# Kernel tuning notes

Measured on AMD Instinct MI355X. Metric: run time of the kernel, lower is better.

The kernel has to match this reference:

```python
import jax, jax.numpy as jnp
import numpy as np

LEAKY = 0.2  # tf.nn.leaky_relu default alpha
E_SZ = [64, 64, 16]
F_SZ = [128, 128, 8]
N_MAPS, C, H, W = 64, 1, 32, 32
B = 8192


def _leaky(x):
    return jnp.where(x >= 0, x, LEAKY * x)


def func_theta(x, theta, sz, in_sz):
    # x: [B, in_sz]; theta: [B, total]; per-sample MLP with weights sliced from theta
    y = x
    offset = 0
    n = len(sz)
    for i, out_sz in enumerate(sz):
        w_sz = in_sz * out_sz
        Wm = theta[:, offset:offset + w_sz].reshape(-1, in_sz, out_sz)
        offset += w_sz
        b = theta[:, offset:offset + out_sz]
        offset += out_sz
        y = jnp.einsum('bi,bio->bo', y, Wm) + b
        if i < n - 1:
            y = _leaky(y)
        in_sz = out_sz
    return y


def setup_inputs() -> dict:
    key = jax.random.key(0)
    ks = jax.random.split(key, 16)

    def g(k, shape, scale):
        return (jax.random.normal(k, shape, dtype=jnp.float32) * scale)

    inp = {
        'indices': jax.random.randint(ks[0], (B,), 0, N_MAPS, dtype=jnp.int32),
        'states': jax.random.normal(ks[1], (B, 4), dtype=jnp.float32),
        'maps': jax.random.normal(ks[2], (N_MAPS, C, H, W), dtype=jnp.float32),
        'fc1_w': g(ks[3], (C * H * W, 256), 1.0 / np.sqrt(C * H * W)),
        'fc1_b': jnp.zeros((256,), jnp.float32),
        'fc2_w': g(ks[4], (256, 128), 1.0 / np.sqrt(256)),
        'fc2_b': jnp.zeros((128,), jnp.float32),
        'fc3_w': g(ks[5], (128, 128), 1.0 / np.sqrt(128)),
        'fc3_b': jnp.zeros((128,), jnp.float32),
        'bn_w': g(ks[6], (128, 32), 1.0 / np.sqrt(128)),
        'bn_b': jnp.zeros((32,), jnp.float32),
        'e_w': g(ks[7], (32, 5456), 1e-5),
        'e_b': g(ks[8], (5456,), 1e-3),
        'f_w': g(ks[9], (32, 21768), 1e-5),
        'f_b': g(ks[10], (21768,), 1e-3),
    }
    return inp


def reference(indices, states, maps, fc1_w, fc1_b, fc2_w, fc2_b, fc3_w, fc3_b,
              bn_w, bn_b, e_w, e_b, f_w, f_b):
    # gather maps per sample and flatten (NCHW -> NHWC transpose is a no-op after flatten
    # mathematically, but keep the exact data layout of the original)
    m = jnp.transpose(maps[indices], (0, 2, 3, 1)).astype(jnp.float32)  # [B,H,W,C]
    z = m.reshape(m.shape[0], -1)

    # hypernet trunk
    z = _leaky(z @ fc1_w + fc1_b)
    z = _leaky(z @ fc2_w + fc2_b)
    z = _leaky(z @ fc3_w + fc3_b)
    z = z @ bn_w + bn_b  # bottleneck, no activation
    theta_e = z @ e_w + e_b  # [B, 5456]
    theta_f = z @ f_w + f_b  # [B, 21768]

    S = states[:, 0:2]
    G = states[:, 2:4]
    e_s = func_theta(S, theta_e, E_SZ, 2)
    e_g = func_theta(G, theta_e, E_SZ, 2)
    zf = jnp.concatenate([e_s, e_g], axis=-1)  # [B, 32]
    ang = func_theta(zf, theta_f, F_SZ, 2 * E_SZ[-1])  # [B, 8]
    pts = jnp.concatenate([jnp.sin(ang), jnp.cos(ang)], axis=-1)  # [B, 16]
    return pts
```

## Files before the change

kernel.cpp:

```cpp
#include <hip/hip_runtime.h>
#include <hip/hip_bf16.h>


#define LEAKY 0.2f
#define NCLS 64
#define B_TOT 8192
#define NSLICE 8
#define EST 68
#define FST 132


__device__ __forceinline__ float lrelu(float x) { return x >= 0.f ? x : LEAKY * x; }

__global__ __launch_bounds__(1024) void backbone_bucket_kernel(
    const float* __restrict__ maps,
    const float* __restrict__ fc1_w, const float* __restrict__ fc1_b,
    const float* __restrict__ fc2_w, const float* __restrict__ fc2_b,
    const float* __restrict__ fc3_w, const float* __restrict__ fc3_b,
    const float* __restrict__ bn_w,  const float* __restrict__ bn_b,
    float* __restrict__ z,
    const int* __restrict__ idx, int* __restrict__ counts,
    int* __restrict__ offsets, int* __restrict__ perm)
{
    __shared__ float m[1024];
    __shared__ __align__(16) float4 red4[1024];
    __shared__ __align__(16) float h1[256];
    __shared__ __align__(16) float h2[128];
    __shared__ __align__(16) float h3[128];
    __shared__ int cnt[16][64];
    __shared__ int wcur[16][64];

    const int t = threadIdx.x;

    if (blockIdx.x == 64) {
        const int w = t >> 6;
        cnt[w][t & 63] = 0;
        __syncthreads();
        int my[8];
#pragma unroll
        for (int r = 0; r < 8; ++r) {
            my[r] = idx[r * 1024 + t];
            atomicAdd(&cnt[w][my[r]], 1);
        }
        __syncthreads();
        if (t < 64) {
            int run = 0;
#pragma unroll
            for (int w2 = 0; w2 < 16; ++w2) {
                const int v = cnt[w2][t];
                wcur[w2][t] = run;
                run += v;
            }
            counts[t] = run;
            int x = run;
            for (int d = 1; d < 64; d <<= 1) {
                const int y = __shfl_up(x, d, 64);
                if (t >= d) x += y;
            }
            const int basec = x - run;
            offsets[t] = basec;
#pragma unroll
            for (int w2 = 0; w2 < 16; ++w2) wcur[w2][t] += basec;
        }
        __syncthreads();
#pragma unroll
        for (int r = 0; r < 8; ++r) {
            const int p = atomicAdd(&wcur[w][my[r]], 1);
            perm[p] = r * 1024 + t;
        }
        return;
    }

    const int c = blockIdx.x;
    m[t] = maps[(size_t)c * 1024 + t];
    __syncthreads();

    {
        const int og = t & 63, ks = t >> 6;
        const float* wp = fc1_w + og * 4;
        float4 acc = {0.f, 0.f, 0.f, 0.f};
#pragma unroll 8
        for (int i = 0; i < 64; ++i) {
            const int k = ks * 64 + i;
            const float mk = m[k];
            const float4 w = *(const float4*)&wp[(size_t)k * 256];
            acc.x += mk * w.x; acc.y += mk * w.y;
            acc.z += mk * w.z; acc.w += mk * w.w;
        }
        red4[t] = acc;
    }
    __syncthreads();
    if (t < 64) {
        float4 a = *(const float4*)&fc1_b[t * 4];
#pragma unroll
        for (int r = 0; r < 16; ++r) {
            const float4 v = red4[r * 64 + t];
            a.x += v.x; a.y += v.y; a.z += v.z; a.w += v.w;
        }
        a.x = lrelu(a.x); a.y = lrelu(a.y); a.z = lrelu(a.z); a.w = lrelu(a.w);
        *(float4*)&h1[t * 4] = a;
    }
    __syncthreads();
    {
        const int og = t & 31, ks = t >> 5;
        float4 acc = {0.f, 0.f, 0.f, 0.f};
#pragma unroll
        for (int i = 0; i < 8; ++i) {
            const int k = ks * 8 + i;
            const float hk = h1[k];
            const float4 w = *(const float4*)&fc2_w[k * 128 + og * 4];
            acc.x += hk * w.x; acc.y += hk * w.y;
            acc.z += hk * w.z; acc.w += hk * w.w;
        }
        red4[t] = acc;
    }
    __syncthreads();
    if (t < 32) {
        float4 a = *(const float4*)&fc2_b[t * 4];
#pragma unroll
        for (int r = 0; r < 32; ++r) {
            const float4 v = red4[r * 32 + t];
            a.x += v.x; a.y += v.y; a.z += v.z; a.w += v.w;
        }
        a.x = lrelu(a.x); a.y = lrelu(a.y); a.z = lrelu(a.z); a.w = lrelu(a.w);
        *(float4*)&h2[t * 4] = a;
    }
    __syncthreads();
    {
        const int og = t & 31, ks = t >> 5;
        float4 acc = {0.f, 0.f, 0.f, 0.f};
#pragma unroll
        for (int i = 0; i < 4; ++i) {
            const int k = ks * 4 + i;
            const float hk = h2[k];
            const float4 w = *(const float4*)&fc3_w[k * 128 + og * 4];
            acc.x += hk * w.x; acc.y += hk * w.y;
            acc.z += hk * w.z; acc.w += hk * w.w;
        }
        red4[t] = acc;
    }
    __syncthreads();
    if (t < 32) {
        float4 a = *(const float4*)&fc3_b[t * 4];
#pragma unroll
        for (int r = 0; r < 32; ++r) {
            const float4 v = red4[r * 32 + t];
            a.x += v.x; a.y += v.y; a.z += v.z; a.w += v.w;
        }
        a.x = lrelu(a.x); a.y = lrelu(a.y); a.z = lrelu(a.z); a.w = lrelu(a.w);
        *(float4*)&h3[t * 4] = a;
    }
    __syncthreads();
    {
        const int og = t & 7, ks = t >> 3;
        const float hk = h3[ks];
        const float4 w = *(const float4*)&bn_w[ks * 32 + og * 4];
        float4 acc;
        acc.x = hk * w.x; acc.y = hk * w.y; acc.z = hk * w.z; acc.w = hk * w.w;
        red4[t] = acc;
    }
    __syncthreads();
    if (t < 8) {
        float4 a = *(const float4*)&bn_b[t * 4];
#pragma unroll
        for (int r = 0; r < 128; ++r) {
            const float4 v = red4[r * 8 + t];
            a.x += v.x; a.y += v.y; a.z += v.z; a.w += v.w;
        }
        *(float4*)&z[c * 32 + t * 4] = a;
    }
}

__global__ __launch_bounds__(256) void theta_kernel(
    const float* __restrict__ z,
    const float* __restrict__ e_w, const float* __restrict__ e_b,
    const float* __restrict__ f_w, const float* __restrict__ f_b,
    float* __restrict__ th_e, float* __restrict__ th_f)
{
    __shared__ __align__(16) float zl[2048];
    const int t = threadIdx.x;
    ((float4*)zl)[t]       = ((const float4*)z)[t];
    ((float4*)zl)[t + 256] = ((const float4*)z)[t + 256];
    __syncthreads();

    int j = blockIdx.x * 256 + t;
    const int cbase = blockIdx.y * 8;
    const float* wbase;
    float* op;
    int stride;
    float bias;
    if (j < 5456) {
        wbase = e_w + j; bias = e_b[j]; op = th_e + j; stride = 5456;
    } else {
        const int jj = j - 5456;
        if (jj >= 21768) return;
        wbase = f_w + jj; bias = f_b[jj]; op = th_f + jj; stride = 21768;
    }
    float wk[32];
#pragma unroll
    for (int k = 0; k < 32; ++k) wk[k] = wbase[(size_t)k * stride];

#pragma unroll
    for (int cc = 0; cc < 8; cc += 4) {
        const int c0 = cbase + cc;
        float a0 = bias, a1 = bias, a2 = bias, a3 = bias;
#pragma unroll
        for (int k4 = 0; k4 < 8; ++k4) {
            const float4 z0 = *(const float4*)&zl[(c0 + 0) * 32 + k4 * 4];
            const float4 z1 = *(const float4*)&zl[(c0 + 1) * 32 + k4 * 4];
            const float4 z2 = *(const float4*)&zl[(c0 + 2) * 32 + k4 * 4];
            const float4 z3 = *(const float4*)&zl[(c0 + 3) * 32 + k4 * 4];
            const float w0 = wk[k4 * 4], w1 = wk[k4 * 4 + 1];
            const float w2 = wk[k4 * 4 + 2], w3 = wk[k4 * 4 + 3];
            a0 += z0.x * w0 + z0.y * w1 + z0.z * w2 + z0.w * w3;
            a1 += z1.x * w0 + z1.y * w1 + z1.z * w2 + z1.w * w3;
            a2 += z2.x * w0 + z2.y * w1 + z2.z * w2 + z2.w * w3;
            a3 += z3.x * w0 + z3.y * w1 + z3.z * w2 + z3.w * w3;
        }
        op[(size_t)(c0 + 0) * stride] = a0;
        op[(size_t)(c0 + 1) * stride] = a1;
        op[(size_t)(c0 + 2) * stride] = a2;
        op[(size_t)(c0 + 3) * stride] = a3;
    }
}

__global__ __launch_bounds__(256, 3) void func_kernel(
    const float* __restrict__ states,
    const float* __restrict__ th_e_all, const float* __restrict__ th_f_all,
    const int* __restrict__ counts, const int* __restrict__ offsets,
    const int* __restrict__ perm, float* __restrict__ out)
{
    __shared__ __align__(16) float wbuf[5392];
    __shared__ __align__(16) float w3fb[1160];
    __shared__ __align__(16) float actA[2176];
    __shared__ __align__(16) float actB[2176];
    __shared__ __align__(16) float part[256];

    const int c = blockIdx.x;
    const int s = blockIdx.y;
    const int nb   = counts[c];
    const int base = offsets[c];
    const int chunk = (nb + NSLICE - 1) / NSLICE;
    const int k0 = s * chunk;
    const int k1 = (nb < k0 + chunk) ? nb : (k0 + chunk);
    const int cntq = (k1 > k0) ? (k1 - k0) : 0;
    if (cntq == 0) return;

    const float* te = th_e_all + (size_t)c * 5456;
    const float* tf = th_f_all + (size_t)c * 21768;

    const int t   = threadIdx.x;
    const int vbs = t & 7;
    const int ce  = (t >> 3) * 2;
    const int vb3 = t & 31;
    const int c3  = (t >> 5) * 2;
    const int fbs = t & 3;
    const int cf  = (t >> 2) * 2;
    const int b3  = t & 15;
    const int c8  = (t >> 4) & 7;
    const int kh  = t >> 7;

    for (int j = t * 4; j < 5392; j += 1024)
        *(float4*)&wbuf[j] = *(const float4*)&te[j];
    for (int j = t * 4; j < 1160; j += 1024)
        *(float4*)&w3fb[j] = *(const float4*)&tf[20608 + j];

    const int passes = (cntq + 15) >> 4;
    for (int p = 0; p < passes; ++p) {
        if (p) {
            __syncthreads();
            for (int j = t * 4; j < 5392; j += 1024)
                *(float4*)&wbuf[j] = *(const float4*)&te[j];
        }
        __syncthreads();

        const int kkA = k0 + p * 16 + vbs;
        const int kkB = kkA + 8;
        const int biA = (kkA < k1) ? perm[base + kkA] : 0;
        const int biB = (kkB < k1) ? perm[base + kkB] : 0;
        const float4 stA = *(const float4*)&states[(size_t)biA * 4];
        const float4 stB = *(const float4*)&states[(size_t)biB * 4];
        const float i0[4] = {stA.x, stB.x, stA.z, stB.z};
        const float i1[4] = {stA.y, stB.y, stA.w, stB.w};

        {
            const float2 wa = *(const float2*)&wbuf[ce];
            const float2 wb = *(const float2*)&wbuf[64 + ce];
            const float2 bb = *(const float2*)&wbuf[128 + ce];
#pragma unroll
            for (int j = 0; j < 4; ++j) {
                float2 o;
                o.x = lrelu(i0[j] * wa.x + i1[j] * wb.x + bb.x);
                o.y = lrelu(i0[j] * wa.y + i1[j] * wb.y + bb.y);
                *(float2*)&actA[(vbs + 8 * j) * EST + ce] = o;
            }
        }
        __syncthreads();

        {
            float a0[4] = {0, 0, 0, 0}, a1[4] = {0, 0, 0, 0};
#pragma unroll 4
            for (int k4 = 0; k4 < 16; ++k4) {
                float4 y[4];
#pragma unroll
                for (int j = 0; j < 4; ++j)
                    y[j] = *(const float4*)&actA[(vbs + 8 * j) * EST + k4 * 4];
#pragma unroll
                for (int u = 0; u < 4; ++u) {
                    const float2 w = *(const float2*)&wbuf[192 + (k4 * 4 + u) * 64 + ce];
#pragma unroll
                    for (int j = 0; j < 4; ++j) {
                        const float yv = (&y[j].x)[u];
                        a0[j] += yv * w.x;
                        a1[j] += yv * w.y;
                    }
                }
            }
            const float2 b2 = *(const float2*)&wbuf[4288 + ce];
#pragma unroll
            for (int j = 0; j < 4; ++j) {
                float2 o;
                o.x = lrelu(a0[j] + b2.x);
                o.y = lrelu(a1[j] + b2.y);
                *(float2*)&actB[(vbs + 8 * j) * EST + ce] = o;
            }
        }
        __syncthreads();

        {
            float a0 = 0.f, a1 = 0.f;
#pragma unroll 4
            for (int k4 = 0; k4 < 16; ++k4) {
                const float4 y = *(const float4*)&actB[vb3 * EST + k4 * 4];
#pragma unroll
                for (int u = 0; u < 4; ++u) {
                    const int i = k4 * 4 + u;
                    a0 += (&y.x)[u] * wbuf[4352 + i * 16 + c3];
                    a1 += (&y.x)[u] * wbuf[4352 + i * 16 + c3 + 1];
                }
            }
            const int fo = (vb3 & 15) * FST + (vb3 >> 4) * 16 + c3;
            actA[fo]     = a0 + wbuf[5376 + c3];
            actA[fo + 1] = a1 + wbuf[5376 + c3 + 1];
        }
        __syncthreads();

        for (int j = t * 4; j < 4224; j += 1024)
            *(float4*)&wbuf[j] = *(const float4*)&tf[j];
        __syncthreads();

        {
            float a0[4] = {0, 0, 0, 0}, a1[4] = {0, 0, 0, 0};
#pragma unroll
            for (int k4 = 0; k4 < 8; ++k4) {
                float4 y[4];
#pragma unroll
                for (int j = 0; j < 4; ++j)
                    y[j] = *(const float4*)&actA[(fbs + 4 * j) * FST + k4 * 4];
#pragma unroll
                for (int u = 0; u < 4; ++u) {
                    const float2 w = *(const float2*)&wbuf[(k4 * 4 + u) * 128 + cf];
#pragma unroll
                    for (int j = 0; j < 4; ++j) {
                        const float yv = (&y[j].x)[u];
                        a0[j] += yv * w.x;
                        a1[j] += yv * w.y;
                    }
                }
            }
            const float2 b1 = *(const float2*)&wbuf[4096 + cf];
#pragma unroll
            for (int j = 0; j < 4; ++j) {
                float2 o;
                o.x = lrelu(a0[j] + b1.x);
                o.y = lrelu(a1[j] + b1.y);
                *(float2*)&actB[(fbs + 4 * j) * FST + cf] = o;
            }
        }
        __syncthreads();

        {
            float a0[4] = {0, 0, 0, 0}, a1[4] = {0, 0, 0, 0};
#pragma unroll
            for (int h = 0; h < 4; ++h) {
                for (int j = t * 4; j < 4096; j += 1024)
                    *(float4*)&wbuf[j] = *(const float4*)&tf[4224 + h * 4096 + j];
                __syncthreads();
#pragma unroll 4
                for (int k4 = 0; k4 < 8; ++k4) {
                    float4 y[4];
#pragma unroll
                    for (int j = 0; j < 4; ++j)
                        y[j] = *(const float4*)&actB[(fbs + 4 * j) * FST + h * 32 + k4 * 4];
#pragma unroll
                    for (int u = 0; u < 4; ++u) {
                        const float2 w = *(const float2*)&wbuf[(k4 * 4 + u) * 128 + cf];
#pragma unroll
                        for (int j = 0; j < 4; ++j) {
                            const float yv = (&y[j].x)[u];
                            a0[j] += yv * w.x;
                            a1[j] += yv * w.y;
                        }
                    }
                }
                __syncthreads();
            }
            const float2 b2 = *(const float2*)&w3fb[cf];
#pragma unroll
            for (int j = 0; j < 4; ++j) {
                float2 o;
                o.x = lrelu(a0[j] + b2.x);
                o.y = lrelu(a1[j] + b2.y);
                *(float2*)&actA[(fbs + 4 * j) * FST + cf] = o;
            }
        }
        __syncthreads();

        {
            float a = 0.f;
#pragma unroll
            for (int k4 = kh * 16; k4 < kh * 16 + 16; ++k4) {
                const float4 y = *(const float4*)&actA[b3 * FST + k4 * 4];
#pragma unroll
                for (int u = 0; u < 4; ++u)
                    a += (&y.x)[u] * w3fb[128 + (k4 * 4 + u) * 8 + c8];
            }
            part[kh * 128 + b3 * 8 + c8] = a;
        }
        __syncthreads();

        if (t < 128) {
            const int bb = t >> 3, cc8 = t & 7;
            const int kk2 = k0 + p * 16 + bb;
            if (kk2 < k1) {
                const int bi2 = perm[base + kk2];
                const float a = part[bb * 8 + cc8] + part[128 + bb * 8 + cc8]
                              + w3fb[1152 + cc8];
                out[(size_t)bi2 * 16 + cc8]     = __sinf(a);
                out[(size_t)bi2 * 16 + 8 + cc8] = __cosf(a);
            }
        }
    }
}

extern "C" void kernel_launch(void* const* d_in, const int* in_sizes, int n_in,
                              void* d_out, int out_size, void* d_ws, size_t ws_size,
                              hipStream_t stream)
{
    const int*   indices = (const int*)  d_in[0];
    const float* states  = (const float*)d_in[1];
    const float* maps    = (const float*)d_in[2];
    const float* fc1_w   = (const float*)d_in[3];
    const float* fc1_b   = (const float*)d_in[4];
    const float* fc2_w   = (const float*)d_in[5];
    const float* fc2_b   = (const float*)d_in[6];
    const float* fc3_w   = (const float*)d_in[7];
    const float* fc3_b   = (const float*)d_in[8];
    const float* bn_w    = (const float*)d_in[9];
    const float* bn_b    = (const float*)d_in[10];
    const float* e_w     = (const float*)d_in[11];
    const float* e_b     = (const float*)d_in[12];
    const float* f_w     = (const float*)d_in[13];
    const float* f_b     = (const float*)d_in[14];
    float* out = (float*)d_out;

    float* ws   = (float*)d_ws;
    float* z    = ws;
    float* th_e = ws + 2048;
    float* th_f = ws + 351232;
    int* counts  = (int*)(ws + 1744384);
    int* offsets = counts + 64;
    int* perm    = counts + 128;

    backbone_bucket_kernel<<<65, 1024, 0, stream>>>(
        maps, fc1_w, fc1_b, fc2_w, fc2_b, fc3_w, fc3_b, bn_w, bn_b, z,
        indices, counts, offsets, perm);
    theta_kernel<<<dim3(107, 8), 256, 0, stream>>>(
        z, e_w, e_b, f_w, f_b, th_e, th_f);
    func_kernel<<<dim3(NCLS, NSLICE), 256, 0, stream>>>(
        states, th_e, th_f, counts, offsets, perm, out);
}
```

Before: 149.7 us.

## Read per-class theta weights directly from global memory instead of staging in LDS

After: 169.6 us. 1.13x slower.

```diff
diff --git a/kernel.cpp b/kernel.cpp
--- a/kernel.cpp
+++ b/kernel.cpp
@@ -5,9 +5,9 @@
 #define LEAKY 0.2f
 #define NCLS 64
 #define B_TOT 8192
-#define NSLICE 8
-#define EST 68
-#define FST 132
+#define NSLICE 16
+#define SESTR 18
+#define SFSTR 10
 
 
 __device__ __forceinline__ float lrelu(float x) { return x >= 0.f ? x : LEAKY * x; }
@@ -224,16 +224,16 @@
     }
 }
 
-__global__ __launch_bounds__(256, 3) void func_kernel(
+__global__ __launch_bounds__(256, 4) void func_kernel(
     const float* __restrict__ states,
     const float* __restrict__ th_e_all, const float* __restrict__ th_f_all,
     const int* __restrict__ counts, const int* __restrict__ offsets,
     const int* __restrict__ perm, float* __restrict__ out)
 {
-    __shared__ __align__(16) float wbuf[5392];
-    __shared__ __align__(16) float w3fb[1160];
-    __shared__ __align__(16) float actA[2176];
-    __shared__ __align__(16) float actB[2176];
+    __shared__ __align__(16) float sE[64 * SESTR];
+    __shared__ __align__(16) float sZ[32 * 8];
+    __shared__ __align__(16) float sF[128 * SFSTR];
+    __shared__ __align__(16) float sG[128 * SFSTR];
     __shared__ __align__(16) float part[256];
 
     const int c = blockIdx.x;
@@ -243,201 +243,123 @@
     const int chunk = (nb + NSLICE - 1) / NSLICE;
     const int k0 = s * chunk;
     const int k1 = (nb < k0 + chunk) ? nb : (k0 + chunk);
-    const int cntq = (k1 > k0) ? (k1 - k0) : 0;
-    if (cntq == 0) return;
+    const int cnt = (k1 > k0) ? (k1 - k0) : 0;
+    if (cnt == 0) return;
 
     const float* te = th_e_all + (size_t)c * 5456;
     const float* tf = th_f_all + (size_t)c * 21768;
 
-    const int t   = threadIdx.x;
-    const int vbs = t & 7;
-    const int ce  = (t >> 3) * 2;
-    const int vb3 = t & 31;
-    const int c3  = (t >> 5) * 2;
-    const int fbs = t & 3;
-    const int cf  = (t >> 2) * 2;
-    const int b3  = t & 15;
-    const int c8  = (t >> 4) & 7;
-    const int kh  = t >> 7;
-
-    for (int j = t * 4; j < 5392; j += 1024)
-        *(float4*)&wbuf[j] = *(const float4*)&te[j];
-    for (int j = t * 4; j < 1160; j += 1024)
-        *(float4*)&w3fb[j] = *(const float4*)&tf[20608 + j];
-
-    const int passes = (cntq + 15) >> 4;
+    const int t = threadIdx.x;
+    const int vb   = t & 15;
+    const int cq   = (t >> 4) * 4;
+    const int vbs2 = (t & 7) * 2;
+    const int ce   = (t >> 3) * 2;
+    const int c3   = t >> 4;
+    const int bs   = t & 3;
+    const int cf   = (t >> 2) * 2;
+    const int b8 = t & 7, c8 = (t >> 3) & 7, kq = t >> 6;
+
+    const int passes = (cnt + 7) >> 3;
     for (int p = 0; p < passes; ++p) {
-        if (p) {
-            __syncthreads();
-            for (int j = t * 4; j < 5392; j += 1024)
-                *(float4*)&wbuf[j] = *(const float4*)&te[j];
-        }
-        __syncthreads();
-
-        const int kkA = k0 + p * 16 + vbs;
-        const int kkB = kkA + 8;
-        const int biA = (kkA < k1) ? perm[base + kkA] : 0;
-        const int biB = (kkB < k1) ? perm[base + kkB] : 0;
-        const float4 stA = *(const float4*)&states[(size_t)biA * 4];
-        const float4 stB = *(const float4*)&states[(size_t)biB * 4];
-        const float i0[4] = {stA.x, stB.x, stA.z, stB.z};
-        const float i1[4] = {stA.y, stB.y, stA.w, stB.w};
-
-        {
-            const float2 wa = *(const float2*)&wbuf[ce];
-            const float2 wb = *(const float2*)&wbuf[64 + ce];
-            const float2 bb = *(const float2*)&wbuf[128 + ce];
-#pragma unroll
-            for (int j = 0; j < 4; ++j) {
-                float2 o;
-                o.x = lrelu(i0[j] * wa.x + i1[j] * wb.x + bb.x);
-                o.y = lrelu(i0[j] * wa.y + i1[j] * wb.y + bb.y);
-                *(float2*)&actA[(vbs + 8 * j) * EST + ce] = o;
-            }
-        }
-        __syncthreads();
-
-        {
-            float a0[4] = {0, 0, 0, 0}, a1[4] = {0, 0, 0, 0};
-#pragma unroll 4
-            for (int k4 = 0; k4 < 16; ++k4) {
-                float4 y[4];
-#pragma unroll
-                for (int j = 0; j < 4; ++j)
-                    y[j] = *(const float4*)&actA[(vbs + 8 * j) * EST + k4 * 4];
-#pragma unroll
-                for (int u = 0; u < 4; ++u) {
-                    const float2 w = *(const float2*)&wbuf[192 + (k4 * 4 + u) * 64 + ce];
-#pragma unroll
-                    for (int j = 0; j < 4; ++j) {
-                        const float yv = (&y[j].x)[u];
-                        a0[j] += yv * w.x;
-                        a1[j] += yv * w.y;
-                    }
-                }
-            }
-            const float2 b2 = *(const float2*)&wbuf[4288 + ce];
-#pragma unroll
-            for (int j = 0; j < 4; ++j) {
-                float2 o;
-                o.x = lrelu(a0[j] + b2.x);
-                o.y = lrelu(a1[j] + b2.y);
-                *(float2*)&actB[(vbs + 8 * j) * EST + ce] = o;
-            }
-        }
-        __syncthreads();
-
-        {
-            float a0 = 0.f, a1 = 0.f;
-#pragma unroll 4
-            for (int k4 = 0; k4 < 16; ++k4) {
-                const float4 y = *(const float4*)&actB[vb3 * EST + k4 * 4];
-#pragma unroll
-                for (int u = 0; u < 4; ++u) {
-                    const int i = k4 * 4 + u;
-                    a0 += (&y.x)[u] * wbuf[4352 + i * 16 + c3];
-                    a1 += (&y.x)[u] * wbuf[4352 + i * 16 + c3 + 1];
-                }
-            }
-            const int fo = (vb3 & 15) * FST + (vb3 >> 4) * 16 + c3;
-            actA[fo]     = a0 + wbuf[5376 + c3];
-            actA[fo + 1] = a1 + wbuf[5376 + c3 + 1];
-        }
-        __syncthreads();
-
-        for (int j = t * 4; j < 4224; j += 1024)
-            *(float4*)&wbuf[j] = *(const float4*)&tf[j];
-        __syncthreads();
-
-        {
-            float a0[4] = {0, 0, 0, 0}, a1[4] = {0, 0, 0, 0};
-#pragma unroll
-            for (int k4 = 0; k4 < 8; ++k4) {
-                float4 y[4];
-#pragma unroll
-                for (int j = 0; j < 4; ++j)
-                    y[j] = *(const float4*)&actA[(fbs + 4 * j) * FST + k4 * 4];
-#pragma unroll
-                for (int u = 0; u < 4; ++u) {
-                    const float2 w = *(const float2*)&wbuf[(k4 * 4 + u) * 128 + cf];
-#pragma unroll
-                    for (int j = 0; j < 4; ++j) {
-                        const float yv = (&y[j].x)[u];
-                        a0[j] += yv * w.x;
-                        a1[j] += yv * w.y;
-                    }
-                }
-            }
-            const float2 b1 = *(const float2*)&wbuf[4096 + cf];
-#pragma unroll
-            for (int j = 0; j < 4; ++j) {
-                float2 o;
-                o.x = lrelu(a0[j] + b1.x);
-                o.y = lrelu(a1[j] + b1.y);
-                *(float2*)&actB[(fbs + 4 * j) * FST + cf] = o;
-            }
-        }
-        __syncthreads();
-
-        {
-            float a0[4] = {0, 0, 0, 0}, a1[4] = {0, 0, 0, 0};
-#pragma unroll
-            for (int h = 0; h < 4; ++h) {
-                for (int j = t * 4; j < 4096; j += 1024)
-                    *(float4*)&wbuf[j] = *(const float4*)&tf[4224 + h * 4096 + j];
-                __syncthreads();
-#pragma unroll 4
-                for (int k4 = 0; k4 < 8; ++k4) {
-                    float4 y[4];
-#pragma unroll
-                    for (int j = 0; j < 4; ++j)
-                        y[j] = *(const float4*)&actB[(fbs + 4 * j) * FST + h * 32 + k4 * 4];
-#pragma unroll
-                    for (int u = 0; u < 4; ++u) {
-                        const float2 w = *(const float2*)&wbuf[(k4 * 4 + u) * 128 + cf];
-#pragma unroll
-                        for (int j = 0; j < 4; ++j) {
-                            const float yv = (&y[j].x)[u];
-                            a0[j] += yv * w.x;
-                            a1[j] += yv * w.y;
-                        }
-                    }
-                }
-                __syncthreads();
-            }
-            const float2 b2 = *(const float2*)&w3fb[cf];
-#pragma unroll
-            for (int j = 0; j < 4; ++j) {
-                float2 o;
-                o.x = lrelu(a0[j] + b2.x);
-                o.y = lrelu(a1[j] + b2.y);
-                *(float2*)&actA[(fbs + 4 * j) * FST + cf] = o;
-            }
-        }
+        if (p) __syncthreads();
+
+        const int kk = k0 + p * 8 + (vb & 7);
+        const int bi = (kk < k1) ? perm[base + kk] : 0;
+        const float2 sv = *(const float2*)&states[(size_t)bi * 4 + (vb >> 3) * 2];
+
+        {
+            const float4 wa = *(const float4*)&te[cq];
+            const float4 wb = *(const float4*)&te[64 + cq];
+            const float4 bb = *(const float4*)&te[128 + cq];
+            sE[(cq + 0) * SESTR + vb] = lrelu(sv.x * wa.x + sv.y * wb.x + bb.x);
+            sE[(cq + 1) * SESTR + vb] = lrelu(sv.x * wa.y + sv.y * wb.y + bb.y);
+            sE[(cq + 2) * SESTR + vb] = lrelu(sv.x * wa.z + sv.y * wb.z + bb.z);
+            sE[(cq + 3) * SESTR + vb] = lrelu(sv.x * wa.w + sv.y * wb.w + bb.w);
+        }
+        __syncthreads();
+
+        float e00, e01, e10, e11;
+        {
+            float a00 = 0, a01 = 0, a10 = 0, a11 = 0;
+#pragma unroll 8
+            for (int k = 0; k < 64; ++k) {
+                const float2 w = *(const float2*)&te[192 + k * 64 + ce];
+                const float2 y = *(const float2*)&sE[k * SESTR + vbs2];
+                a00 += y.x * w.x; a01 += y.x * w.y;
+                a10 += y.y * w.x; a11 += y.y * w.y;
+            }
+            const float2 b2 = *(const float2*)&te[4288 + ce];
+            e00 = lrelu(a00 + b2.x); e01 = lrelu(a01 + b2.y);
+            e10 = lrelu(a10 + b2.x); e11 = lrelu(a11 + b2.y);
+        }
+        __syncthreads();
+        *(float2*)&sE[(ce + 0) * SESTR + vbs2] = float2{e00, e10};
+        *(float2*)&sE[(ce + 1) * SESTR + vbs2] = float2{e01, e11};
         __syncthreads();
 
         {
             float a = 0.f;
-#pragma unroll
-            for (int k4 = kh * 16; k4 < kh * 16 + 16; ++k4) {
-                const float4 y = *(const float4*)&actA[b3 * FST + k4 * 4];
-#pragma unroll
-                for (int u = 0; u < 4; ++u)
-                    a += (&y.x)[u] * w3fb[128 + (k4 * 4 + u) * 8 + c8];
-            }
-            part[kh * 128 + b3 * 8 + c8] = a;
-        }
-        __syncthreads();
-
-        if (t < 128) {
-            const int bb = t >> 3, cc8 = t & 7;
-            const int kk2 = k0 + p * 16 + bb;
+#pragma unroll 8
+            for (int k = 0; k < 64; ++k)
+                a += sE[k * SESTR + vb] * te[4352 + k * 16 + c3];
+            a += te[5376 + c3];
+            sZ[((vb >> 3) * 16 + c3) * 8 + (vb & 7)] = a;
+        }
+        __syncthreads();
+
+        {
+            float a00 = 0, a01 = 0, a10 = 0, a11 = 0;
+#pragma unroll 8
+            for (int k = 0; k < 32; ++k) {
+                const float2 w = *(const float2*)&tf[k * 128 + cf];
+                const float2 y = *(const float2*)&sZ[k * 8 + bs * 2];
+                a00 += y.x * w.x; a01 += y.x * w.y;
+                a10 += y.y * w.x; a11 += y.y * w.y;
+            }
+            const float2 b1 = *(const float2*)&tf[4096 + cf];
+            *(float2*)&sF[(cf + 0) * SFSTR + bs * 2] =
+                float2{lrelu(a00 + b1.x), lrelu(a10 + b1.x)};
+            *(float2*)&sF[(cf + 1) * SFSTR + bs * 2] =
+                float2{lrelu(a01 + b1.y), lrelu(a11 + b1.y)};
+        }
+        __syncthreads();
+
+        {
+            float a00 = 0, a01 = 0, a10 = 0, a11 = 0;
+#pragma unroll 8
+            for (int k = 0; k < 128; ++k) {
+                const float2 w = *(const float2*)&tf[4224 + k * 128 + cf];
+                const float2 y = *(const float2*)&sF[k * SFSTR + bs * 2];
+                a00 += y.x * w.x; a01 += y.x * w.y;
+                a10 += y.y * w.x; a11 += y.y * w.y;
+            }
+            const float2 b2 = *(const float2*)&tf[20608 + cf];
+            *(float2*)&sG[(cf + 0) * SFSTR + bs * 2] =
+                float2{lrelu(a00 + b2.x), lrelu(a10 + b2.x)};
+            *(float2*)&sG[(cf + 1) * SFSTR + bs * 2] =
+                float2{lrelu(a01 + b2.y), lrelu(a11 + b2.y)};
+        }
+        __syncthreads();
+
+        {
+            float a = 0.f;
+#pragma unroll 8
+            for (int k = kq * 32; k < kq * 32 + 32; ++k)
+                a += sG[k * SFSTR + b8] * tf[20736 + k * 8 + c8];
+            part[kq * 64 + b8 * 8 + c8] = a;
+        }
+        __syncthreads();
+
+        if (t < 64) {
+            const int bb = t >> 3, cc = t & 7;
+            const int kk2 = k0 + p * 8 + bb;
             if (kk2 < k1) {
                 const int bi2 = perm[base + kk2];
-                const float a = part[bb * 8 + cc8] + part[128 + bb * 8 + cc8]
-                              + w3fb[1152 + cc8];
-                out[(size_t)bi2 * 16 + cc8]     = __sinf(a);
-                out[(size_t)bi2 * 16 + 8 + cc8] = __cosf(a);
+                const float a = part[bb * 8 + cc] + part[64 + bb * 8 + cc]
+                              + part[128 + bb * 8 + cc] + part[192 + bb * 8 + cc]
+                              + tf[21760 + cc];
+                out[(size_t)bi2 * 16 + cc]     = __sinf(a);
+                out[(size_t)bi2 * 16 + 8 + cc] = __cosf(a);
             }
         }
     }
```
